# Performance work log

Hardware: AMD Instinct MI355X
Metric: run time of the kernel (lower is better)

The kernel has to match this reference:

```python
import jax, jax.numpy as jnp
import numpy as np

H = 18  # hidden/input size hardcoded in the module
B, T = 1024, 1024

def _uniform(key, shape, scale):
    return jax.random.uniform(key, shape, jnp.float32, -scale, scale)

def setup_inputs() -> dict:
    key = jax.random.key(0)
    ks = jax.random.split(key, 12)
    s = 1.0 / np.sqrt(H)
    x = jax.random.normal(ks[0], (B, T, H), dtype=jnp.float32)
    return {
        "x": x,
        "gru_Wih": _uniform(ks[1], (3 * H, H), s),
        "gru_Whh": _uniform(ks[2], (3 * H, H), s),
        "gru_bih": _uniform(ks[3], (3 * H,), s),
        "gru_bhh": _uniform(ks[4], (3 * H,), s),
        "lstm_Wih": _uniform(ks[5], (4 * H, H), s),
        "lstm_Whh": _uniform(ks[6], (4 * H, H), s),
        "lstm_bih": _uniform(ks[7], (4 * H,), s),
        "lstm_bhh": _uniform(ks[8], (4 * H,), s),
        "fc_W": _uniform(ks[9], (1, H), s),
        "fc_b": _uniform(ks[10], (1,), s),
    }

def _gru(x, Wih, Whh, bih, bhh):
    # x: [B, T, H]. Precompute input contributions for all timesteps.
    xi = jnp.einsum("bth,gh->btg", x, Wih) + bih  # [B, T, 3H]
    xi_t = jnp.transpose(xi, (1, 0, 2))            # [T, B, 3H]
    h0 = jnp.zeros((x.shape[0], H), x.dtype)

    def step(h, xt):
        hh = h @ Whh.T + bhh                        # [B, 3H]
        xr, xz, xn = jnp.split(xt, 3, axis=-1)
        hr, hz, hn = jnp.split(hh, 3, axis=-1)
        r = jax.nn.sigmoid(xr + hr)
        z = jax.nn.sigmoid(xz + hz)
        n = jnp.tanh(xn + r * hn)
        h_new = (1.0 - z) * n + z * h
        return h_new, h_new

    _, hs = jax.lax.scan(step, h0, xi_t)
    return jnp.transpose(hs, (1, 0, 2))             # [B, T, H]

def _lstm(x, Wih, Whh, bih, bhh):
    xi = jnp.einsum("bth,gh->btg", x, Wih) + bih   # [B, T, 4H]
    xi_t = jnp.transpose(xi, (1, 0, 2))
    h0 = jnp.zeros((x.shape[0], H), x.dtype)
    c0 = jnp.zeros((x.shape[0], H), x.dtype)

    def step(carry, xt):
        h, c = carry
        g = xt + h @ Whh.T + bhh                    # [B, 4H]
        i, f, gg, o = jnp.split(g, 4, axis=-1)      # PyTorch gate order i,f,g,o
        i = jax.nn.sigmoid(i)
        f = jax.nn.sigmoid(f)
        gg = jnp.tanh(gg)
        o = jax.nn.sigmoid(o)
        c_new = f * c + i * gg
        h_new = o * jnp.tanh(c_new)
        return (h_new, c_new), h_new

    _, hs = jax.lax.scan(step, (h0, c0), xi_t)
    return jnp.transpose(hs, (1, 0, 2))

def reference(x, gru_Wih, gru_Whh, gru_bih, gru_bhh,
              lstm_Wih, lstm_Whh, lstm_bih, lstm_bhh, fc_W, fc_b):
    g = _gru(x, gru_Wih, gru_Whh, gru_bih, gru_bhh)
    l = _lstm(g, lstm_Wih, lstm_Whh, lstm_bih, lstm_bhh)
    return jnp.einsum("bth,oh->bto", l, fc_W) + fc_b  # [B, T, 1]
```

## Files before the change

### kernel.cpp

```cpp
#include <hip/hip_runtime.h>
#include <cstdint>
#include <cstddef>
#include <math.h>

#define LC 1.44269504088896340736f

__device__ __forceinline__ float rl_(float v, int k) {
    return __int_as_float(__builtin_amdgcn_readlane(__float_as_int(v), k));
}
__device__ __forceinline__ float bp_(float v, int addr4) {
    return __int_as_float(__builtin_amdgcn_ds_bpermute(addr4, __float_as_int(v)));
}
#define SZ_(v, pat) __int_as_float(__builtin_amdgcn_ds_swizzle(__float_as_int(v), (pat)))

__device__ __forceinline__ float sigm_(float u) {
    return __fdividef(1.f, 1.f + exp2f(-LC * u));
}
__device__ __forceinline__ float tanh_(float u) {
    return fmaf(-2.f, __fdividef(1.f, 1.f + exp2f((2.f * LC) * u)), 1.f);
}
__device__ __forceinline__ void ld18_(float* d, const float* s) {
    *(float4*)&d[0]  = *(const float4*)&s[0];
    *(float4*)&d[4]  = *(const float4*)&s[4];
    *(float4*)&d[8]  = *(const float4*)&s[8];
    *(float4*)&d[12] = *(const float4*)&s[12];
    d[16] = s[16]; d[17] = s[17];
}

__global__ __launch_bounds__(256) void rnn_fused8(
    const float* __restrict__ x,
    const float* __restrict__ gWih, const float* __restrict__ gWhh,
    const float* __restrict__ gbih, const float* __restrict__ gbhh,
    const float* __restrict__ lWih, const float* __restrict__ lWhh,
    const float* __restrict__ lbih, const float* __restrict__ lbhh,
    const float* __restrict__ fcW, const float* __restrict__ fcb,
    float* __restrict__ out)
{
    const int tid  = threadIdx.x;
    const int wid  = tid >> 6;
    const int lane = tid & 63;
    const int b    = blockIdx.x;
    const int role = (wid + b) & 3;

    __shared__ __align__(16) float xaR[16][64];
    __shared__ __align__(16) float hR [16][64];
    __shared__ __align__(16) float xlR[16][80];
    __shared__ __align__(16) float xst[2][8][20];

    const float* xb   = x   + (size_t)b * (1024 * 18);
    float*       outp = out + (size_t)b * 1024;

    const bool sec  = (lane >= 54) && (lane < 62);
    const int  rg   = (lane < 54) ? lane : 0;
    const int  rsec = sec ? (64 + lane - 54) : 64;

    if (role == 3) {
        float wX[18];
        #pragma unroll
        for (int k = 0; k < 18; k++) wX[k] = (lane < 54) ? gWih[rg * 18 + k] : 0.f;
        const float bX = (lane < 54) ? gbih[rg] : 0.f;

        const int j0 = lane, j1 = lane + 64, j2 = lane + 128;
        const int r0 = j0 / 18, c0 = j0 % 18;
        const int r1 = j1 / 18, c1 = j1 % 18;
        const int r2 = j2 / 18, c2 = j2 % 18;

        float p0 = xb[j0], p1 = xb[j1], p2 = (lane < 16) ? xb[j2] : 0.f;
        xst[0][r0][c0] = p0; xst[0][r1][c1] = p1; if (lane < 16) xst[0][r2][c2] = p2;
        __builtin_amdgcn_wave_barrier();
        #pragma unroll
        for (int j = 0; j < 8; j++) {
            float xr[18]; ld18_(xr, &xst[0][j][0]);
            float a0 = bX, a1 = 0.f;
            #pragma unroll
            for (int k = 0; k < 18; k += 2) { a0 = fmaf(wX[k], xr[k], a0); a1 = fmaf(wX[k+1], xr[k+1], a1); }
            xaR[j][lane] = a0 + a1;
        }
        p0 = xb[144 + j0]; p1 = xb[144 + j1]; if (lane < 16) p2 = xb[144 + j2];

        for (int p = 0; p < 130; p++) {
            __syncthreads();
            if (p <= 126) {
                const int bu = (p + 1) & 1;
                xst[bu][r0][c0] = p0; xst[bu][r1][c1] = p1; if (lane < 16) xst[bu][r2][c2] = p2;
                if (p + 2 <= 127) {
                    const float* xw = xb + (size_t)(p + 2) * 144;
                    p0 = xw[j0]; p1 = xw[j1]; if (lane < 16) p2 = xw[j2];
                }
                __builtin_amdgcn_wave_barrier();
                const int s1 = ((p + 1) * 8) & 15;
                #pragma unroll
                for (int j = 0; j < 8; j++) {
                    float xr[18]; ld18_(xr, &xst[bu][j][0]);
                    float a0 = bX, a1 = 0.f;
                    #pragma unroll
                    for (int k = 0; k < 18; k += 2) { a0 = fmaf(wX[k], xr[k], a0); a1 = fmaf(wX[k+1], xr[k+1], a1); }
                    xaR[s1 + j][lane] = a0 + a1;
                }
            }
        }
    } else if (role == 0) {
        float wG[18];
        #pragma unroll
        for (int k = 0; k < 18; k++) wG[k] = (lane < 54) ? gWhh[rg * 18 + k] : 0.f;
        const float bG = (lane < 54) ? gbhh[rg] : 0.f;

        const int i1b = ((lane + 18) & 63) << 2;
        const int i2b = ((lane + 36) & 63) << 2;
        const int i3b = ((lane + 28) & 63) << 2;

        float myh = 0.f;

        for (int p = 0; p < 130; p++) {
            __syncthreads();
            if (p <= 127) {
                const int s0 = (p * 8) & 15;
                #pragma unroll
                for (int j = 0; j < 8; j++) {
                    const float xa = xaR[s0 + j][lane];
                    float a0 = bG, a1 = 0.f;
                    #pragma unroll
                    for (int k = 0; k < 18; k += 2) {
                        const float s_0 = rl_(myh, k), s_1 = rl_(myh, k + 1);
                        a0 = fmaf(wG[k], s_0, a0); a1 = fmaf(wG[k+1], s_1, a1);
                    }
                    const float ha = a0 + a1;
                    const float sg = sigm_(xa + ha);
                    const float rv = bp_(sg, i3b);
                    const float tn = tanh_(fmaf(rv, ha, xa));
                    const float zz = bp_(sg, i1b);
                    const float nn = bp_(tn, i2b);
                    myh = fmaf(zz, myh - nn, nn);
                    hR[s0 + j][lane] = myh;
                }
            }
        }
    } else if (role == 1) {
        float wP[18], wS[18];
        #pragma unroll
        for (int k = 0; k < 18; k++) {
            wP[k] = lWih[lane * 18 + k];
            wS[k] = sec ? lWih[rsec * 18 + k] : 0.f;
        }
        const float bP = lbih[lane];
        const float bS = sec ? lbih[rsec] : 0.f;

        for (int p = 0; p < 130; p++) {
            __syncthreads();
            if (p >= 1 && p <= 128) {
                const int s0 = ((p - 1) * 8) & 15;
                #pragma unroll
                for (int j = 0; j < 8; j++) {
                    const float hreg = hR[s0 + j][lane];
                    float a0 = bP, a1 = 0.f, c0 = bS, c1 = 0.f;
                    #pragma unroll
                    for (int k = 0; k < 18; k += 2) {
                        const float s_0 = rl_(hreg, k), s_1 = rl_(hreg, k + 1);
                        a0 = fmaf(wP[k], s_0, a0); a1 = fmaf(wP[k+1], s_1, a1);
                        c0 = fmaf(wS[k], s_0, c0); c1 = fmaf(wS[k+1], s_1, c1);
                    }
                    xlR[s0 + j][lane] = a0 + a1;
                    if (sec) xlR[s0 + j][64 + (lane - 54)] = c0 + c1;
                }
            }
        }
    } else {
        float wL[18], wL2[18];
        #pragma unroll
        for (int k = 0; k < 18; k++) {
            wL[k]  = lWhh[lane * 18 + k];
            wL2[k] = sec ? lWhh[rsec * 18 + k] : 0.f;
        }
        const float bL  = lbhh[lane];
        const float bL2 = sec ? lbhh[rsec] : 0.f;

        const int i1b = ((lane + 18) & 63) << 2;
        const int i2b = ((lane + 36) & 63) << 2;
        const int i3b = ((lane + 54) & 63) << 2;
        const int i4b = ((lane + 44) & 63) << 2;

        const bool  isg = (lane >= 36) && (lane < 54);
        const float kl  = isg ? (2.f * LC) : LC;
        const float Aa  = isg ? 2.f : 1.f;
        const float Bb  = isg ? -1.f : 0.f;

        const float fcw  = (lane < 18) ? fcW[lane] : 0.f;
        const float fcbv = fcb[0];

        float myc = 0.f, myhl = 0.f;
        float o0 = 0.f, o1 = 0.f, o2 = 0.f, o3 = 0.f;

        for (int p = 0; p < 130; p++) {
            __syncthreads();
            if (p >= 2) {
                const int base = (p - 2) * 8;
                const int s0   = base & 15;
                #pragma unroll
                for (int j = 0; j < 8; j++) {
                    const float xl  = xlR[s0 + j][lane];
                    const float xl2 = xlR[s0 + j][64 + ((lane - 54) & 7)];
                    float a0 = bL, a1 = 0.f, c0 = bL2, c1 = 0.f;
                    #pragma unroll
                    for (int k = 0; k < 18; k += 2) {
                        const float s_0 = rl_(myhl, k), s_1 = rl_(myhl, k + 1);
                        a0 = fmaf(wL[k], s_0, a0); a1 = fmaf(wL[k+1], s_1, a1);
                        c0 = fmaf(wL2[k], s_0, c0); c1 = fmaf(wL2[k+1], s_1, c1);
                    }
                    const float a3 = fmaf(Aa, __fdividef(1.f, 1.f + exp2f(-kl * (xl + a0 + a1))), Bb);
                    const float a4 = sigm_(xl2 + c0 + c1);
                    const float ff = bp_(a3, i1b);
                    const float gg = bp_(a3, i2b);
                    const float oa = bp_(a3, i3b);
                    const float ob = bp_(a4, i4b);
                    const float oo = (lane < 10) ? oa : ob;
                    myc  = fmaf(ff, myc, a3 * gg);
                    myhl = oo * tanh_(myc);
                    float fv = fcw * myhl;
                    fv += SZ_(fv, 0x041F); fv += SZ_(fv, 0x081F);
                    fv += SZ_(fv, 0x101F); fv += SZ_(fv, 0x201F); fv += SZ_(fv, 0x401F);
                    const float ov = fv + fcbv;
                    if ((j & 3) == 0) o0 = ov; else if ((j & 3) == 1) o1 = ov;
                    else if ((j & 3) == 2) o2 = ov; else o3 = ov;
                    if ((j & 3) == 3 && lane == 0) {
                        float4 vv; vv.x = o0; vv.y = o1; vv.z = o2; vv.w = o3;
                        *reinterpret_cast<float4*>(outp + base + j - 3) = vv;
                    }
                }
            }
        }
    }
}

extern "C" void kernel_launch(void* const* d_in, const int* in_sizes, int n_in,
                              void* d_out, int out_size, void* d_ws, size_t ws_size,
                              hipStream_t stream)
{
    (void)d_ws; (void)ws_size; (void)in_sizes; (void)n_in; (void)out_size;
    const float* xx   = (const float*)d_in[0];
    const float* gWih = (const float*)d_in[1];
    const float* gWhh = (const float*)d_in[2];
    const float* gbih = (const float*)d_in[3];
    const float* gbhh = (const float*)d_in[4];
    const float* lWih = (const float*)d_in[5];
    const float* lWhh = (const float*)d_in[6];
    const float* lbih = (const float*)d_in[7];
    const float* lbhh = (const float*)d_in[8];
    const float* fcW  = (const float*)d_in[9];
    const float* fcb  = (const float*)d_in[10];
    float* outp = (float*)d_out;

    dim3 grid(1024), block(256);
    hipLaunchKernelGGL(rnn_fused8, grid, block, 0, stream,
                       xx, gWih, gWhh, gbih, gbhh,
                       lWih, lWhh, lbih, lbhh, fcW, fcb, outp);
}
```

Measured before the change: 562.7 us.

## Move FC head to input-projection wave and shorten recurrent critical paths

The final FC reduction and output store move out of the LSTM recurrence wave into the GRU input-projection wave, which now reads LSTM hidden states from a new shared buffer one stage later. The pipeline gains one extra stage. The GRU and LSTM recurrent steps permute pre-activations before applying the nonlinearities, so the permutes no longer wait on the transcendental results. The LSTM input-projection wave reads h vectors straight from LDS instead of using readlane, and the recurrent waves raise their scheduling priority. This costs more LDS, an extra pipeline iteration, and redundant transcendental evaluations per lane.

```diff
diff --git a/kernel.cpp b/kernel.cpp
--- a/kernel.cpp
+++ b/kernel.cpp
@@ -27,7 +27,7 @@
     d[16] = s[16]; d[17] = s[17];
 }
 
-__global__ __launch_bounds__(256) void rnn_fused8(
+__global__ __launch_bounds__(256) void rnn_fused9(
     const float* __restrict__ x,
     const float* __restrict__ gWih, const float* __restrict__ gWhh,
     const float* __restrict__ gbih, const float* __restrict__ gbhh,
@@ -44,7 +44,8 @@
 
     __shared__ __align__(16) float xaR[16][64];
     __shared__ __align__(16) float hR [16][64];
-    __shared__ __align__(16) float xlR[16][80];
+    __shared__ __align__(16) float xlR[32][80];
+    __shared__ __align__(16) float hlR[16][64];
     __shared__ __align__(16) float xst[2][8][20];
 
     const float* xb   = x   + (size_t)b * (1024 * 18);
@@ -58,12 +59,16 @@
         float wX[18];
         #pragma unroll
         for (int k = 0; k < 18; k++) wX[k] = (lane < 54) ? gWih[rg * 18 + k] : 0.f;
-        const float bX = (lane < 54) ? gbih[rg] : 0.f;
+        const float bX   = (lane < 54) ? gbih[rg] : 0.f;
+        const float fcw  = (lane < 18) ? fcW[lane] : 0.f;
+        const float fcbv = fcb[0];
 
         const int j0 = lane, j1 = lane + 64, j2 = lane + 128;
         const int r0 = j0 / 18, c0 = j0 % 18;
         const int r1 = j1 / 18, c1 = j1 % 18;
         const int r2 = j2 / 18, c2 = j2 % 18;
+
+        float o0 = 0.f, o1 = 0.f, o2 = 0.f, o3 = 0.f;
 
         float p0 = xb[j0], p1 = xb[j1], p2 = (lane < 16) ? xb[j2] : 0.f;
         xst[0][r0][c0] = p0; xst[0][r1][c1] = p1; if (lane < 16) xst[0][r2][c2] = p2;
@@ -78,7 +83,7 @@
         }
         p0 = xb[144 + j0]; p1 = xb[144 + j1]; if (lane < 16) p2 = xb[144 + j2];
 
-        for (int p = 0; p < 130; p++) {
+        for (int p = 0; p < 131; p++) {
             __syncthreads();
             if (p <= 126) {
                 const int bu = (p + 1) & 1;
@@ -98,124 +103,13 @@
                     xaR[s1 + j][lane] = a0 + a1;
                 }
             }
-        }
-    } else if (role == 0) {
-        float wG[18];
-        #pragma unroll
-        for (int k = 0; k < 18; k++) wG[k] = (lane < 54) ? gWhh[rg * 18 + k] : 0.f;
-        const float bG = (lane < 54) ? gbhh[rg] : 0.f;
-
-        const int i1b = ((lane + 18) & 63) << 2;
-        const int i2b = ((lane + 36) & 63) << 2;
-        const int i3b = ((lane + 28) & 63) << 2;
-
-        float myh = 0.f;
-
-        for (int p = 0; p < 130; p++) {
-            __syncthreads();
-            if (p <= 127) {
-                const int s0 = (p * 8) & 15;
-                #pragma unroll
-                for (int j = 0; j < 8; j++) {
-                    const float xa = xaR[s0 + j][lane];
-                    float a0 = bG, a1 = 0.f;
-                    #pragma unroll
-                    for (int k = 0; k < 18; k += 2) {
-                        const float s_0 = rl_(myh, k), s_1 = rl_(myh, k + 1);
-                        a0 = fmaf(wG[k], s_0, a0); a1 = fmaf(wG[k+1], s_1, a1);
-                    }
-                    const float ha = a0 + a1;
-                    const float sg = sigm_(xa + ha);
-                    const float rv = bp_(sg, i3b);
-                    const float tn = tanh_(fmaf(rv, ha, xa));
-                    const float zz = bp_(sg, i1b);
-                    const float nn = bp_(tn, i2b);
-                    myh = fmaf(zz, myh - nn, nn);
-                    hR[s0 + j][lane] = myh;
-                }
-            }
-        }
-    } else if (role == 1) {
-        float wP[18], wS[18];
-        #pragma unroll
-        for (int k = 0; k < 18; k++) {
-            wP[k] = lWih[lane * 18 + k];
-            wS[k] = sec ? lWih[rsec * 18 + k] : 0.f;
-        }
-        const float bP = lbih[lane];
-        const float bS = sec ? lbih[rsec] : 0.f;
-
-        for (int p = 0; p < 130; p++) {
-            __syncthreads();
-            if (p >= 1 && p <= 128) {
-                const int s0 = ((p - 1) * 8) & 15;
-                #pragma unroll
-                for (int j = 0; j < 8; j++) {
-                    const float hreg = hR[s0 + j][lane];
-                    float a0 = bP, a1 = 0.f, c0 = bS, c1 = 0.f;
-                    #pragma unroll
-                    for (int k = 0; k < 18; k += 2) {
-                        const float s_0 = rl_(hreg, k), s_1 = rl_(hreg, k + 1);
-                        a0 = fmaf(wP[k], s_0, a0); a1 = fmaf(wP[k+1], s_1, a1);
-                        c0 = fmaf(wS[k], s_0, c0); c1 = fmaf(wS[k+1], s_1, c1);
-                    }
-                    xlR[s0 + j][lane] = a0 + a1;
-                    if (sec) xlR[s0 + j][64 + (lane - 54)] = c0 + c1;
-                }
-            }
-        }
-    } else {
-        float wL[18], wL2[18];
-        #pragma unroll
-        for (int k = 0; k < 18; k++) {
-            wL[k]  = lWhh[lane * 18 + k];
-            wL2[k] = sec ? lWhh[rsec * 18 + k] : 0.f;
-        }
-        const float bL  = lbhh[lane];
-        const float bL2 = sec ? lbhh[rsec] : 0.f;
-
-        const int i1b = ((lane + 18) & 63) << 2;
-        const int i2b = ((lane + 36) & 63) << 2;
-        const int i3b = ((lane + 54) & 63) << 2;
-        const int i4b = ((lane + 44) & 63) << 2;
-
-        const bool  isg = (lane >= 36) && (lane < 54);
-        const float kl  = isg ? (2.f * LC) : LC;
-        const float Aa  = isg ? 2.f : 1.f;
-        const float Bb  = isg ? -1.f : 0.f;
-
-        const float fcw  = (lane < 18) ? fcW[lane] : 0.f;
-        const float fcbv = fcb[0];
-
-        float myc = 0.f, myhl = 0.f;
-        float o0 = 0.f, o1 = 0.f, o2 = 0.f, o3 = 0.f;
-
-        for (int p = 0; p < 130; p++) {
-            __syncthreads();
-            if (p >= 2) {
-                const int base = (p - 2) * 8;
-                const int s0   = base & 15;
-                #pragma unroll
-                for (int j = 0; j < 8; j++) {
-                    const float xl  = xlR[s0 + j][lane];
-                    const float xl2 = xlR[s0 + j][64 + ((lane - 54) & 7)];
-                    float a0 = bL, a1 = 0.f, c0 = bL2, c1 = 0.f;
-                    #pragma unroll
-                    for (int k = 0; k < 18; k += 2) {
-                        const float s_0 = rl_(myhl, k), s_1 = rl_(myhl, k + 1);
-                        a0 = fmaf(wL[k], s_0, a0); a1 = fmaf(wL[k+1], s_1, a1);
-                        c0 = fmaf(wL2[k], s_0, c0); c1 = fmaf(wL2[k+1], s_1, c1);
-                    }
-                    const float a3 = fmaf(Aa, __fdividef(1.f, 1.f + exp2f(-kl * (xl + a0 + a1))), Bb);
-                    const float a4 = sigm_(xl2 + c0 + c1);
-                    const float ff = bp_(a3, i1b);
-                    const float gg = bp_(a3, i2b);
-                    const float oa = bp_(a3, i3b);
-                    const float ob = bp_(a4, i4b);
-                    const float oo = (lane < 10) ? oa : ob;
-                    myc  = fmaf(ff, myc, a3 * gg);
-                    myhl = oo * tanh_(myc);
-                    float fv = fcw * myhl;
+            if (p >= 3) {
+                const int base = (p - 3) * 8;
+                const int s    = base & 15;
+                #pragma unroll
+                for (int j = 0; j < 8; j++) {
+                    const float hlv = hlR[s + j][lane];
+                    float fv = fcw * hlv;
                     fv += SZ_(fv, 0x041F); fv += SZ_(fv, 0x081F);
                     fv += SZ_(fv, 0x101F); fv += SZ_(fv, 0x201F); fv += SZ_(fv, 0x401F);
                     const float ov = fv + fcbv;
@@ -226,6 +120,126 @@
                         *reinterpret_cast<float4*>(outp + base + j - 3) = vv;
                     }
                 }
+            }
+        }
+    } else if (role == 0) {
+        float wG[18];
+        #pragma unroll
+        for (int k = 0; k < 18; k++) wG[k] = (lane < 54) ? gWhh[rg * 18 + k] : 0.f;
+        const float bG = (lane < 54) ? gbhh[rg] : 0.f;
+
+        const int ibx = ((lane + 36) & 63) << 2;
+        const int ibz = ((lane + 18) & 63) << 2;
+
+        float myh = 0.f;
+
+        for (int p = 0; p < 131; p++) {
+            __syncthreads();
+            if (p <= 127) {
+                const int s0 = (p * 8) & 15;
+                __builtin_amdgcn_s_setprio(1);
+                #pragma unroll
+                for (int j = 0; j < 8; j++) {
+                    const float xa = xaR[s0 + j][lane];
+                    float a0 = bG, a1 = 0.f;
+                    #pragma unroll
+                    for (int k = 0; k < 18; k += 2) {
+                        const float s_0 = rl_(myh, k), s_1 = rl_(myh, k + 1);
+                        a0 = fmaf(wG[k], s_0, a0); a1 = fmaf(wG[k+1], s_1, a1);
+                    }
+                    const float ha  = a0 + a1;
+                    const float bpx = bp_(xa, ibx);
+                    const float bph = bp_(ha, ibx);
+                    const float sg  = sigm_(xa + ha);
+                    const float zz  = bp_(sg, ibz);
+                    const float nv  = tanh_(fmaf(sg, bph, bpx));
+                    myh = fmaf(zz, myh - nv, nv);
+                    hR[s0 + j][lane] = myh;
+                }
+                __builtin_amdgcn_s_setprio(0);
+            }
+        }
+    } else if (role == 1) {
+        float wP[18], wS[18];
+        #pragma unroll
+        for (int k = 0; k < 18; k++) {
+            wP[k] = lWih[lane * 18 + k];
+            wS[k] = sec ? lWih[rsec * 18 + k] : 0.f;
+        }
+        const float bP = lbih[lane];
+        const float bS = sec ? lbih[rsec] : 0.f;
+
+        for (int p = 0; p < 131; p++) {
+            __syncthreads();
+            if (p >= 1 && p <= 128) {
+                const int base = (p - 1) * 8;
+                const int s0   = base & 15;
+                #pragma unroll
+                for (int j = 0; j < 8; j++) {
+                    float hv[18]; ld18_(hv, &hR[s0 + j][0]);
+                    float a0 = bP, a1 = 0.f, c0 = bS, c1 = 0.f;
+                    #pragma unroll
+                    for (int k = 0; k < 18; k += 2) {
+                        a0 = fmaf(wP[k],   hv[k],   a0); a1 = fmaf(wP[k+1], hv[k+1], a1);
+                        c0 = fmaf(wS[k],   hv[k],   c0); c1 = fmaf(wS[k+1], hv[k+1], c1);
+                    }
+                    const int sl = (base + j) & 31;
+                    xlR[sl][lane] = a0 + a1;
+                    if (sec) xlR[sl][64 + (lane - 54)] = c0 + c1;
+                }
+            }
+        }
+    } else {
+        float wL[18], wL2[18];
+        #pragma unroll
+        for (int k = 0; k < 18; k++) {
+            wL[k]  = lWhh[lane * 18 + k];
+            wL2[k] = sec ? lWhh[rsec * 18 + k] : 0.f;
+        }
+        const float bL  = lbhh[lane];
+        const float bL2 = sec ? lbhh[rsec] : 0.f;
+
+        const int ibf  = ((lane + 18) & 63) << 2;
+        const int ibg  = ((lane + 36) & 63) << 2;
+        const int ibo1 = ((lane + 54) & 63) << 2;
+        const int ibo2 = ((lane + 44) & 63) << 2;
+
+        float myc = 0.f, myhl = 0.f;
+
+        for (int p = 0; p < 131; p++) {
+            __syncthreads();
+            if (p >= 2 && p <= 129) {
+                const int base = (p - 2) * 8;
+                const int s0   = base & 15;
+                __builtin_amdgcn_s_setprio(1);
+                #pragma unroll
+                for (int j = 0; j < 8; j++) {
+                    const int sl = (base + j) & 31;
+                    const float xl  = xlR[sl][lane];
+                    const float xl2 = xlR[sl][64 + ((lane - 54) & 7)];
+                    float a0 = bL, a1 = 0.f, c0 = bL2, c1 = 0.f;
+                    #pragma unroll
+                    for (int k = 0; k < 18; k += 2) {
+                        const float s_0 = rl_(myhl, k), s_1 = rl_(myhl, k + 1);
+                        a0 = fmaf(wL[k],  s_0, a0); a1 = fmaf(wL[k+1],  s_1, a1);
+                        c0 = fmaf(wL2[k], s_0, c0); c1 = fmaf(wL2[k+1], s_1, c1);
+                    }
+                    const float pv  = xl + a0 + a1;
+                    const float pv2 = xl2 + c0 + c1;
+                    const float bpf = bp_(pv,  ibf);
+                    const float bpg = bp_(pv,  ibg);
+                    const float bo1 = bp_(pv,  ibo1);
+                    const float bo2 = bp_(pv2, ibo2);
+                    const float po  = (lane < 10) ? bo1 : bo2;
+                    const float iv  = sigm_(pv);
+                    const float fv_ = sigm_(bpf);
+                    const float gv  = tanh_(bpg);
+                    const float ov_ = sigm_(po);
+                    myc  = fmaf(fv_, myc, iv * gv);
+                    myhl = ov_ * tanh_(myc);
+                    hlR[(base + j) & 15][lane] = myhl;
+                }
+                __builtin_amdgcn_s_setprio(0);
             }
         }
     }
@@ -250,7 +264,7 @@
     float* outp = (float*)d_out;
 
     dim3 grid(1024), block(256);
-    hipLaunchKernelGGL(rnn_fused8, grid, block, 0, stream,
+    hipLaunchKernelGGL(rnn_fused9, grid, block, 0, stream,
                        xx, gWih, gWhh, gbih, gbhh,
                        lWih, lWhh, lbih, lbhh, fcW, fcb, outp);
 }
```

After: 684.5 us. 1.22x slower.

## Offload FC reduction to input-projection wave and use packed FMA dot products

Applied to the files above, without the earlier changes.

Moves the final FC reduction and output store out of the LSTM recurrence wave into the otherwise lightly loaded input-projection wave, passing LSTM hidden states through a new shared buffer and extending the pipeline by one stage. The non-recurrent dot products (GRU input projection, LSTM input projection) switch to v_pk_fma_f32 on f2 pairs with vector LDS loads instead of readlane broadcasts. Launch bounds also request 4 blocks per CU. This shortens the critical LSTM chain and halves FMA issue count for the projections, at the cost of extra LDS traffic, one more barrier iteration, and inline asm that may hinder scheduling.

```diff
diff --git a/kernel.cpp b/kernel.cpp
--- a/kernel.cpp
+++ b/kernel.cpp
@@ -5,6 +5,8 @@
 
 #define LC 1.44269504088896340736f
 
+typedef float f2 __attribute__((ext_vector_type(2)));
+
 __device__ __forceinline__ float rl_(float v, int k) {
     return __int_as_float(__builtin_amdgcn_readlane(__float_as_int(v), k));
 }
@@ -18,6 +20,16 @@
 }
 __device__ __forceinline__ float tanh_(float u) {
     return fmaf(-2.f, __fdividef(1.f, 1.f + exp2f((2.f * LC) * u)), 1.f);
+}
+__device__ __forceinline__ void pk_(f2& acc, f2 w, f2 h) {
+    asm("v_pk_fma_f32 %0, %1, %2, %0" : "+v"(acc) : "v"(w), "v"(h));
+}
+__device__ __forceinline__ void ld9p_(f2* d, const float* s) {
+    *(float4*)&d[0] = *(const float4*)&s[0];
+    *(float4*)&d[2] = *(const float4*)&s[4];
+    *(float4*)&d[4] = *(const float4*)&s[8];
+    *(float4*)&d[6] = *(const float4*)&s[12];
+    d[8] = *(const f2*)&s[16];
 }
 __device__ __forceinline__ void ld18_(float* d, const float* s) {
     *(float4*)&d[0]  = *(const float4*)&s[0];
@@ -27,7 +39,7 @@
     d[16] = s[16]; d[17] = s[17];
 }
 
-__global__ __launch_bounds__(256) void rnn_fused8(
+__global__ __launch_bounds__(256, 4) void rnn_fused11(
     const float* __restrict__ x,
     const float* __restrict__ gWih, const float* __restrict__ gWhh,
     const float* __restrict__ gbih, const float* __restrict__ gbhh,
@@ -45,6 +57,7 @@
     __shared__ __align__(16) float xaR[16][64];
     __shared__ __align__(16) float hR [16][64];
     __shared__ __align__(16) float xlR[16][80];
+    __shared__ __align__(16) float hlR[16][64];
     __shared__ __align__(16) float xst[2][8][20];
 
     const float* xb   = x   + (size_t)b * (1024 * 18);
@@ -55,30 +68,38 @@
     const int  rsec = sec ? (64 + lane - 54) : 64;
 
     if (role == 3) {
-        float wX[18];
-        #pragma unroll
-        for (int k = 0; k < 18; k++) wX[k] = (lane < 54) ? gWih[rg * 18 + k] : 0.f;
-        const float bX = (lane < 54) ? gbih[rg] : 0.f;
+        f2 wX2[9];
+        #pragma unroll
+        for (int i = 0; i < 9; i++) {
+            wX2[i].x = (lane < 54) ? gWih[rg * 18 + 2 * i]     : 0.f;
+            wX2[i].y = (lane < 54) ? gWih[rg * 18 + 2 * i + 1] : 0.f;
+        }
+        const float bX   = (lane < 54) ? gbih[rg] : 0.f;
+        const float fcw  = (lane < 18) ? fcW[lane] : 0.f;
+        const float fcbv = fcb[0];
 
         const int j0 = lane, j1 = lane + 64, j2 = lane + 128;
         const int r0 = j0 / 18, c0 = j0 % 18;
         const int r1 = j1 / 18, c1 = j1 % 18;
         const int r2 = j2 / 18, c2 = j2 % 18;
 
+        float o0 = 0.f, o1 = 0.f, o2 = 0.f, o3 = 0.f;
+
         float p0 = xb[j0], p1 = xb[j1], p2 = (lane < 16) ? xb[j2] : 0.f;
         xst[0][r0][c0] = p0; xst[0][r1][c1] = p1; if (lane < 16) xst[0][r2][c2] = p2;
         __builtin_amdgcn_wave_barrier();
         #pragma unroll
         for (int j = 0; j < 8; j++) {
-            float xr[18]; ld18_(xr, &xst[0][j][0]);
-            float a0 = bX, a1 = 0.f;
+            __align__(16) f2 xv[10];
+            ld9p_(xv, &xst[0][j][0]);
+            f2 ax; ax.x = bX; ax.y = 0.f;
             #pragma unroll
-            for (int k = 0; k < 18; k += 2) { a0 = fmaf(wX[k], xr[k], a0); a1 = fmaf(wX[k+1], xr[k+1], a1); }
-            xaR[j][lane] = a0 + a1;
+            for (int i = 0; i < 9; i++) pk_(ax, wX2[i], xv[i]);
+            xaR[j][lane] = ax.x + ax.y;
         }
         p0 = xb[144 + j0]; p1 = xb[144 + j1]; if (lane < 16) p2 = xb[144 + j2];
 
-        for (int p = 0; p < 130; p++) {
+        for (int p = 0; p < 131; p++) {
             __syncthreads();
             if (p <= 126) {
                 const int bu = (p + 1) & 1;
@@ -91,11 +112,30 @@
                 const int s1 = ((p + 1) * 8) & 15;
                 #pragma unroll
                 for (int j = 0; j < 8; j++) {
-                    float xr[18]; ld18_(xr, &xst[bu][j][0]);
-                    float a0 = bX, a1 = 0.f;
-                    #pragma unroll
-                    for (int k = 0; k < 18; k += 2) { a0 = fmaf(wX[k], xr[k], a0); a1 = fmaf(wX[k+1], xr[k+1], a1); }
-                    xaR[s1 + j][lane] = a0 + a1;
+                    __align__(16) f2 xv[10];
+                    ld9p_(xv, &xst[bu][j][0]);
+                    f2 ax; ax.x = bX; ax.y = 0.f;
+                    #pragma unroll
+                    for (int i = 0; i < 9; i++) pk_(ax, wX2[i], xv[i]);
+                    xaR[s1 + j][lane] = ax.x + ax.y;
+                }
+            }
+            if (p >= 3) {
+                const int base = (p - 3) * 8;
+                const int s    = base & 15;
+                #pragma unroll
+                for (int j = 0; j < 8; j++) {
+                    const float hlv = hlR[s + j][lane];
+                    float fv = fcw * hlv;
+                    fv += SZ_(fv, 0x041F); fv += SZ_(fv, 0x081F);
+                    fv += SZ_(fv, 0x101F); fv += SZ_(fv, 0x201F); fv += SZ_(fv, 0x401F);
+                    const float ov = fv + fcbv;
+                    if ((j & 3) == 0) o0 = ov; else if ((j & 3) == 1) o1 = ov;
+                    else if ((j & 3) == 2) o2 = ov; else o3 = ov;
+                    if ((j & 3) == 3 && lane == 0) {
+                        float4 vv; vv.x = o0; vv.y = o1; vv.z = o2; vv.w = o3;
+                        *reinterpret_cast<float4*>(outp + base + j - 3) = vv;
+                    }
                 }
             }
         }
@@ -111,7 +151,7 @@
 
         float myh = 0.f;
 
-        for (int p = 0; p < 130; p++) {
+        for (int p = 0; p < 131; p++) {
             __syncthreads();
             if (p <= 127) {
                 const int s0 = (p * 8) & 15;
@@ -136,31 +176,31 @@
             }
         }
     } else if (role == 1) {
-        float wP[18], wS[18];
-        #pragma unroll
-        for (int k = 0; k < 18; k++) {
-            wP[k] = lWih[lane * 18 + k];
-            wS[k] = sec ? lWih[rsec * 18 + k] : 0.f;
+        f2 wP2[9], wS2[9];
+        #pragma unroll
+        for (int i = 0; i < 9; i++) {
+            wP2[i].x = lWih[lane * 18 + 2 * i];
+            wP2[i].y = lWih[lane * 18 + 2 * i + 1];
+            wS2[i].x = sec ? lWih[rsec * 18 + 2 * i]     : 0.f;
+            wS2[i].y = sec ? lWih[rsec * 18 + 2 * i + 1] : 0.f;
         }
         const float bP = lbih[lane];
         const float bS = sec ? lbih[rsec] : 0.f;
 
-        for (int p = 0; p < 130; p++) {
+        for (int p = 0; p < 131; p++) {
             __syncthreads();
             if (p >= 1 && p <= 128) {
                 const int s0 = ((p - 1) * 8) & 15;
                 #pragma unroll
                 for (int j = 0; j < 8; j++) {
-                    const float hreg = hR[s0 + j][lane];
-                    float a0 = bP, a1 = 0.f, c0 = bS, c1 = 0.f;
-                    #pragma unroll
-                    for (int k = 0; k < 18; k += 2) {
-                        const float s_0 = rl_(hreg, k), s_1 = rl_(hreg, k + 1);
-                        a0 = fmaf(wP[k], s_0, a0); a1 = fmaf(wP[k+1], s_1, a1);
-                        c0 = fmaf(wS[k], s_0, c0); c1 = fmaf(wS[k+1], s_1, c1);
-                    }
-                    xlR[s0 + j][lane] = a0 + a1;
-                    if (sec) xlR[s0 + j][64 + (lane - 54)] = c0 + c1;
+                    __align__(16) f2 hv[10];
+                    ld9p_(hv, &hR[s0 + j][0]);
+                    f2 aP; aP.x = bP; aP.y = 0.f;
+                    f2 aS; aS.x = bS; aS.y = 0.f;
+                    #pragma unroll
+                    for (int i = 0; i < 9; i++) { pk_(aP, wP2[i], hv[i]); pk_(aS, wS2[i], hv[i]); }
+                    xlR[s0 + j][lane] = aP.x + aP.y;
+                    if (sec) xlR[s0 + j][64 + (lane - 54)] = aS.x + aS.y;
                 }
             }
         }
@@ -184,15 +224,11 @@
         const float Aa  = isg ? 2.f : 1.f;
         const float Bb  = isg ? -1.f : 0.f;
 
-        const float fcw  = (lane < 18) ? fcW[lane] : 0.f;
-        const float fcbv = fcb[0];
-
         float myc = 0.f, myhl = 0.f;
-        float o0 = 0.f, o1 = 0.f, o2 = 0.f, o3 = 0.f;
-
-        for (int p = 0; p < 130; p++) {
-            __syncthreads();
-            if (p >= 2) {
+
+        for (int p = 0; p < 131; p++) {
+            __syncthreads();
+            if (p >= 2 && p <= 129) {
                 const int base = (p - 2) * 8;
                 const int s0   = base & 15;
                 #pragma unroll
@@ -215,16 +251,7 @@
                     const float oo = (lane < 10) ? oa : ob;
                     myc  = fmaf(ff, myc, a3 * gg);
                     myhl = oo * tanh_(myc);
-                    float fv = fcw * myhl;
-                    fv += SZ_(fv, 0x041F); fv += SZ_(fv, 0x081F);
-                    fv += SZ_(fv, 0x101F); fv += SZ_(fv, 0x201F); fv += SZ_(fv, 0x401F);
-                    const float ov = fv + fcbv;
-                    if ((j & 3) == 0) o0 = ov; else if ((j & 3) == 1) o1 = ov;
-                    else if ((j & 3) == 2) o2 = ov; else o3 = ov;
-                    if ((j & 3) == 3 && lane == 0) {
-                        float4 vv; vv.x = o0; vv.y = o1; vv.z = o2; vv.w = o3;
-                        *reinterpret_cast<float4*>(outp + base + j - 3) = vv;
-                    }
+                    hlR[s0 + j][lane] = myhl;
                 }
             }
         }
@@ -250,7 +277,7 @@
     float* outp = (float*)d_out;
 
     dim3 grid(1024), block(256);
-    hipLaunchKernelGGL(rnn_fused8, grid, block, 0, stream,
+    hipLaunchKernelGGL(rnn_fused11, grid, block, 0, stream,
                        xx, gWih, gWhh, gbih, gbhh,
                        lWih, lWhh, lbih, lbhh, fcW, fcb, outp);
 }
```

Result: slower. 577.9 us (+2.7%).
